# Kernel tuning notes

Hardware: AMD Instinct MI355X
Metric: run time of the kernel (lower is better)

The kernel has to match this reference:

```python
import jax, jax.numpy as jnp
import numpy as np

DIM = 384
WS = 7
NH = 12
N = WS * WS
B_ = 4096
HEAD_DIM = DIM // NH
SCALE = HEAD_DIM ** (-0.5)


def _relative_position_index(ws: int) -> np.ndarray:
    coords = np.stack(np.meshgrid(np.arange(ws), np.arange(ws), indexing='ij'))  # [2,ws,ws]
    cf = coords.reshape(2, -1)  # [2, N]
    rel = cf[:, :, None] - cf[:, None, :]  # [2, N, N]
    rel = rel.transpose(1, 2, 0).copy()
    rel[:, :, 0] += ws - 1
    rel[:, :, 1] += ws - 1
    rel[:, :, 0] *= 2 * ws - 1
    return rel.sum(-1).astype(np.int32)  # [N, N]


def setup_inputs() -> dict:
    key = jax.random.key(0)
    ks = jax.random.split(key, 6)
    x = jax.random.normal(ks[0], (B_, N, DIM), dtype=jnp.float32)
    qkv_w = jax.random.normal(ks[1], (3 * DIM, DIM), dtype=jnp.float32) * 0.02
    qkv_b = jnp.zeros((3 * DIM,), dtype=jnp.float32)
    proj_w = jax.random.normal(ks[2], (DIM, DIM), dtype=jnp.float32) * 0.02
    proj_b = jnp.zeros((DIM,), dtype=jnp.float32)
    bias_table = jax.random.normal(ks[3], ((2 * WS - 1) * (2 * WS - 1), NH), dtype=jnp.float32) * 0.02
    rel_index = jnp.asarray(_relative_position_index(WS))  # [N, N] int32
    return {"x": x, "qkv_w": qkv_w, "qkv_b": qkv_b, "proj_w": proj_w,
            "proj_b": proj_b, "bias_table": bias_table, "rel_index": rel_index}


def reference(x, qkv_w, qkv_b, proj_w, proj_b, bias_table, rel_index):
    b, n, c = x.shape
    qkv = x @ qkv_w.T + qkv_b  # [B_, N, 3C]
    qkv = qkv.reshape(b, n, 3, NH, HEAD_DIM).transpose(2, 0, 3, 1, 4)  # [3, B_, H, N, hd]
    q, k, v = qkv[0], qkv[1], qkv[2]
    q = q * SCALE
    attn = jnp.einsum('bhnd,bhmd->bhnm', q, k)  # [B_, H, N, N]
    # relative position bias gather: [N*N] -> [N, N, H] -> [H, N, N]
    bias = bias_table[rel_index.reshape(-1)].reshape(n, n, NH).transpose(2, 0, 1)
    attn = attn + bias[None]
    attn = jax.nn.softmax(attn, axis=-1)
    out = jnp.einsum('bhnm,bhmd->bhnd', attn, v)  # [B_, H, N, hd]
    out = out.transpose(0, 2, 1, 3).reshape(b, n, c)
    return out @ proj_w.T + proj_b
```

## Files before the change

kernel.cpp:

```cpp
#include <hip/hip_runtime.h>
#include <stdint.h>
#include <stddef.h>

#define DIM_C    384
#define NHEADS   12
#define SEQ      49
#define HEADD    32
#define NWIN     4096
#define MTOT     (NWIN * SEQ)
#define QKV_N    (3 * DIM_C)
#define ATTN_SCALE 0.17677669529663687f

typedef __bf16 bf16_t;
typedef __bf16 bf16x8 __attribute__((ext_vector_type(8)));
typedef __bf16 bf16x4 __attribute__((ext_vector_type(4)));
typedef float  f32x4  __attribute__((ext_vector_type(4)));

static_assert(sizeof(bf16x8) == 16, "bf16x8 must be 16B");

#define QKV_BYTES     ((size_t)MTOT * QKV_N * 2)
#define AOUT_BYTES    ((size_t)MTOT * DIM_C * 2)
#define BIAS_ELEMS    (NHEADS * SEQ * SEQ)
#define BIASF_BYTES   ((size_t)BIAS_ELEMS * 4)
#define QKVW_BF_BYTES ((size_t)QKV_N * DIM_C * 2)

__global__ void convert_f32_bf16_kernel(const float* __restrict__ src,
                                        bf16_t* __restrict__ dst, int n4) {
    int i = blockIdx.x * 256 + threadIdx.x;
    if (i < n4) {
        float4 v = ((const float4*)src)[i];
        bf16x4 t;
        t[0] = (bf16_t)v.x; t[1] = (bf16_t)v.y;
        t[2] = (bf16_t)v.z; t[3] = (bf16_t)v.w;
        ((bf16x4*)dst)[i] = t;
    }
}

__global__ void bias_expand_kernel(const float* __restrict__ table,
                                   const int* __restrict__ rel,
                                   float* __restrict__ bias_full) {
    int i = blockIdx.x * 256 + threadIdx.x;
    if (i < BIAS_ELEMS) {
        int h  = i / (SEQ * SEQ);
        int mn = i % (SEQ * SEQ);
        bias_full[i] = table[rel[mn] * NHEADS + h];
    }
}

template <bool A_BF16, bool OUT_BF16, int NT>
__global__ __launch_bounds__(256) void gemm_kernel(
    const void* __restrict__ Av, const bf16_t* __restrict__ Bw,
    const float* __restrict__ bias, void* __restrict__ Cv, int ldc) {
    __shared__ bf16_t As[128 * 40];
    __shared__ bf16_t Bs[128 * 40];

    const int tid  = threadIdx.x;
    const int lane = tid & 63;
    const int wave = tid >> 6;
    const int l15  = lane & 15;
    const int quad = lane >> 4;
    const int wm = (wave >> 1) * 64;
    const int wn = (wave & 1) * 64;

    const int cpx = gridDim.x >> 3;
    const int bid = blockIdx.x;
    const int wid = (bid & 7) * cpx + (bid >> 3);
    const size_t m0 = (size_t)(wid / NT) * 128;
    const int    n0 = (wid % NT) * 128;

    f32x4 acc[4][4];
#pragma unroll
    for (int i = 0; i < 4; i++)
#pragma unroll
        for (int j = 0; j < 4; j++) acc[i][j] = f32x4{0.f, 0.f, 0.f, 0.f};

    for (int kt = 0; kt < DIM_C / 32; ++kt) {
        const int k0 = kt * 32;
        __syncthreads();
        if constexpr (A_BF16) {
            const bf16_t* A = (const bf16_t*)Av;
#pragma unroll
            for (int i = 0; i < 2; i++) {
                int c = tid + i * 256;
                int row = c >> 2, kq = c & 3;
                bf16x8 v = *(const bf16x8*)(A + (m0 + row) * DIM_C + k0 + kq * 8);
                *(bf16x8*)(&As[row * 40 + kq * 8]) = v;
            }
        } else {
            const float* A = (const float*)Av;
#pragma unroll
            for (int i = 0; i < 4; i++) {
                int c = tid + i * 256;
                int row = c >> 3, kq = c & 7;
                float4 v = *(const float4*)(A + (m0 + row) * DIM_C + k0 + kq * 4);
                bf16x4 t;
                t[0] = (bf16_t)v.x; t[1] = (bf16_t)v.y;
                t[2] = (bf16_t)v.z; t[3] = (bf16_t)v.w;
                *(bf16x4*)(&As[row * 40 + kq * 4]) = t;
            }
        }
        {
#pragma unroll
            for (int i = 0; i < 2; i++) {
                int c = tid + i * 256;
                int row = c >> 2, kq = c & 3;
                bf16x8 v = *(const bf16x8*)(Bw + (size_t)(n0 + row) * DIM_C + k0 + kq * 8);
                *(bf16x8*)(&Bs[row * 40 + kq * 8]) = v;
            }
        }
        __syncthreads();
        bf16x8 af[4], bfr[4];
#pragma unroll
        for (int mi = 0; mi < 4; mi++)
            af[mi] = *(const bf16x8*)(&As[(wm + mi * 16 + l15) * 40 + quad * 8]);
#pragma unroll
        for (int ni = 0; ni < 4; ni++)
            bfr[ni] = *(const bf16x8*)(&Bs[(wn + ni * 16 + l15) * 40 + quad * 8]);
#pragma unroll
        for (int mi = 0; mi < 4; mi++)
#pragma unroll
            for (int ni = 0; ni < 4; ni++)
                acc[mi][ni] = __builtin_amdgcn_mfma_f32_16x16x32_bf16(
                    af[mi], bfr[ni], acc[mi][ni], 0, 0, 0);
    }
#pragma unroll
    for (int mi = 0; mi < 4; mi++) {
#pragma unroll
        for (int ni = 0; ni < 4; ni++) {
            int col = n0 + wn + ni * 16 + l15;
            float bc = bias[col];
#pragma unroll
            for (int r = 0; r < 4; r++) {
                size_t row = m0 + wm + mi * 16 + quad * 4 + r;
                float v = acc[mi][ni][r] + bc;
                if constexpr (OUT_BF16)
                    ((bf16_t*)Cv)[row * (size_t)ldc + col] = (bf16_t)v;
                else
                    ((float*)Cv)[row * (size_t)ldc + col] = v;
            }
        }
    }
}

__global__ __launch_bounds__(256) void attn_kernel(
    const bf16_t* __restrict__ qkv, const float* __restrict__ bias_full,
    bf16_t* __restrict__ aout) {
    __shared__ bf16_t Ps[4][64 * 72];

    const int b    = blockIdx.x;
    const int lane = threadIdx.x & 63;
    const int wave = threadIdx.x >> 6;
    const int l15  = lane & 15;
    const int quad = lane >> 4;
    const bf16_t* base = qkv + (size_t)b * SEQ * QKV_N;
    bf16_t* ps = &Ps[wave][0];

#pragma unroll 1
    for (int hi = 0; hi < 3; ++hi) {
        const int h = wave * 3 + hi;
        bf16x8 qf[4], kf[4];
#pragma unroll
        for (int mi = 0; mi < 4; mi++) {
            int row = mi * 16 + l15;
            if (row < SEQ) {
                qf[mi] = *(const bf16x8*)(base + (size_t)row * QKV_N + h * HEADD + quad * 8);
                kf[mi] = *(const bf16x8*)(base + (size_t)row * QKV_N + DIM_C + h * HEADD + quad * 8);
            } else {
                bf16x8 z;
#pragma unroll
                for (int j = 0; j < 8; j++) z[j] = (bf16_t)0.f;
                qf[mi] = z; kf[mi] = z;
            }
        }
        f32x4 S[4][4];
#pragma unroll
        for (int mi = 0; mi < 4; mi++)
#pragma unroll
            for (int ni = 0; ni < 4; ni++)
                S[mi][ni] = __builtin_amdgcn_mfma_f32_16x16x32_bf16(
                    qf[mi], kf[ni], f32x4{0.f, 0.f, 0.f, 0.f}, 0, 0, 0);
        const float* bh = bias_full + h * SEQ * SEQ;
#pragma unroll
        for (int mi = 0; mi < 4; mi++)
#pragma unroll
            for (int r = 0; r < 4; r++) {
                int m = mi * 16 + quad * 4 + r;
#pragma unroll
                for (int ni = 0; ni < 4; ni++) {
                    int n = ni * 16 + l15;
                    float s = S[mi][ni][r];
                    s = (m < SEQ && n < SEQ) ? s * ATTN_SCALE + bh[m * SEQ + n] : -1e30f;
                    S[mi][ni][r] = s;
                }
            }
#pragma unroll
        for (int mi = 0; mi < 4; mi++)
#pragma unroll
            for (int r = 0; r < 4; r++) {
                float mx = -1e30f;
#pragma unroll
                for (int ni = 0; ni < 4; ni++) mx = fmaxf(mx, S[mi][ni][r]);
#pragma unroll
                for (int off = 1; off < 16; off <<= 1)
                    mx = fmaxf(mx, __shfl_xor(mx, off, 64));
                float sum = 0.f;
#pragma unroll
                for (int ni = 0; ni < 4; ni++) {
                    float e = __expf(S[mi][ni][r] - mx);
                    S[mi][ni][r] = e;
                    sum += e;
                }
#pragma unroll
                for (int off = 1; off < 16; off <<= 1)
                    sum += __shfl_xor(sum, off, 64);
                float inv = 1.f / sum;
                int m = mi * 16 + quad * 4 + r;
#pragma unroll
                for (int ni = 0; ni < 4; ni++) {
                    int n = ni * 16 + l15;
                    ps[m * 72 + n] = (bf16_t)(S[mi][ni][r] * inv);
                }
            }
        bf16x8 vf[2][2];
#pragma unroll
        for (int ki = 0; ki < 2; ki++)
#pragma unroll
            for (int di = 0; di < 2; di++) {
#pragma unroll
                for (int j = 0; j < 8; j++) {
                    int k = ki * 32 + quad * 8 + j;
                    vf[ki][di][j] = (k < SEQ)
                        ? base[(size_t)k * QKV_N + 2 * DIM_C + h * HEADD + di * 16 + l15]
                        : (bf16_t)0.f;
                }
            }
        f32x4 O[4][2];
#pragma unroll
        for (int mi = 0; mi < 4; mi++)
#pragma unroll
            for (int di = 0; di < 2; di++) O[mi][di] = f32x4{0.f, 0.f, 0.f, 0.f};
#pragma unroll
        for (int mi = 0; mi < 4; mi++)
#pragma unroll
            for (int ki = 0; ki < 2; ki++) {
                bf16x8 pa = *(const bf16x8*)(ps + (mi * 16 + l15) * 72 + ki * 32 + quad * 8);
#pragma unroll
                for (int di = 0; di < 2; di++)
                    O[mi][di] = __builtin_amdgcn_mfma_f32_16x16x32_bf16(
                        pa, vf[ki][di], O[mi][di], 0, 0, 0);
            }
#pragma unroll
        for (int mi = 0; mi < 4; mi++)
#pragma unroll
            for (int di = 0; di < 2; di++)
#pragma unroll
                for (int r = 0; r < 4; r++) {
                    int m = mi * 16 + quad * 4 + r;
                    if (m < SEQ)
                        aout[((size_t)b * SEQ + m) * DIM_C + h * HEADD + di * 16 + l15] =
                            (bf16_t)O[mi][di][r];
                }
    }
}

extern "C" void kernel_launch(void* const* d_in, const int* in_sizes, int n_in,
                              void* d_out, int out_size, void* d_ws, size_t ws_size,
                              hipStream_t stream) {
    (void)in_sizes; (void)n_in; (void)out_size; (void)ws_size;
    const float* x      = (const float*)d_in[0];
    const float* qkv_w  = (const float*)d_in[1];
    const float* qkv_b  = (const float*)d_in[2];
    const float* proj_w = (const float*)d_in[3];
    const float* proj_b = (const float*)d_in[4];
    const float* btable = (const float*)d_in[5];
    const int*   rel    = (const int*)d_in[6];
    float* out = (float*)d_out;

    char* ws = (char*)d_ws;
    bf16_t* qkv        = (bf16_t*)ws;
    bf16_t* aout       = (bf16_t*)(ws + QKV_BYTES);
    float*  bias_full  = (float*)(ws + QKV_BYTES + AOUT_BYTES);
    bf16_t* qkv_w_bf   = (bf16_t*)(ws + QKV_BYTES + AOUT_BYTES + BIASF_BYTES);
    bf16_t* proj_w_bf  = (bf16_t*)(ws + QKV_BYTES + AOUT_BYTES + BIASF_BYTES + QKVW_BF_BYTES);

    convert_f32_bf16_kernel<<<(QKV_N * DIM_C / 4 + 255) / 256, 256, 0, stream>>>(
        qkv_w, qkv_w_bf, QKV_N * DIM_C / 4);
    convert_f32_bf16_kernel<<<(DIM_C * DIM_C / 4 + 255) / 256, 256, 0, stream>>>(
        proj_w, proj_w_bf, DIM_C * DIM_C / 4);
    bias_expand_kernel<<<(BIAS_ELEMS + 255) / 256, 256, 0, stream>>>(btable, rel, bias_full);

    gemm_kernel<false, true, QKV_N / 128><<<(MTOT / 128) * (QKV_N / 128), 256, 0, stream>>>(
        x, qkv_w_bf, qkv_b, qkv, QKV_N);
    attn_kernel<<<NWIN, 256, 0, stream>>>(qkv, bias_full, aout);
    gemm_kernel<true, false, DIM_C / 128><<<(MTOT / 128) * (DIM_C / 128), 256, 0, stream>>>(
        aout, proj_w_bf, proj_b, out, DIM_C);
}
```

Measured before the change: 1.476 ms.

## Write V transposed from QKV GEMM and map one wave per window-head

The QKV GEMM epilogue now writes Q and K to a compact 768-wide buffer and writes V transposed per window into a padded [window][channel][64] layout. That buffer is stored in the output allocation, and its padding positions are zeroed. The attention kernel now gives each wave one (window, head) pair across a swizzled grid instead of three heads per block. It loads V with vector reads instead of scalar strided gathers, and reads the relative-position bias from a pre-padded, fragment-ordered table with the mask folded in. The aim is to cut uncoalesced V loads and per-element bias and mask work, and to raise parallelism. The cost is scattered 2-byte stores in the GEMM epilogue and reuse of the output buffer as scratch.

```diff
diff --git a/kernel.cpp b/kernel.cpp
--- a/kernel.cpp
+++ b/kernel.cpp
@@ -18,10 +18,10 @@
 
 static_assert(sizeof(bf16x8) == 16, "bf16x8 must be 16B");
 
-#define QKV_BYTES     ((size_t)MTOT * QKV_N * 2)
+#define QK_BYTES      ((size_t)MTOT * 768 * 2)
+#define VT_BYTES      ((size_t)NWIN * 384 * 64 * 2)
 #define AOUT_BYTES    ((size_t)MTOT * DIM_C * 2)
-#define BIAS_ELEMS    (NHEADS * SEQ * SEQ)
-#define BIASF_BYTES   ((size_t)BIAS_ELEMS * 4)
+#define BIASL_BYTES   ((size_t)NHEADS * 64 * 64 * 4)
 #define QKVW_BF_BYTES ((size_t)QKV_N * DIM_C * 2)
 
 __global__ void convert_f32_bf16_kernel(const float* __restrict__ src,
@@ -38,19 +38,24 @@
 
 __global__ void bias_expand_kernel(const float* __restrict__ table,
                                    const int* __restrict__ rel,
-                                   float* __restrict__ bias_full) {
+                                   float* __restrict__ bias_l) {
     int i = blockIdx.x * 256 + threadIdx.x;
-    if (i < BIAS_ELEMS) {
-        int h  = i / (SEQ * SEQ);
-        int mn = i % (SEQ * SEQ);
-        bias_full[i] = table[rel[mn] * NHEADS + h];
-    }
-}
-
-template <bool A_BF16, bool OUT_BF16, int NT>
+    if (i < NHEADS * 64 * 64) {
+        int h  = i >> 12;
+        int mn = i & 4095;
+        int m = mn >> 6, n = mn & 63;
+        float v = -1e30f;
+        if (m < SEQ && n < SEQ) v = table[rel[m * SEQ + n] * NHEADS + h];
+        int l = n & 15, ni = n >> 4;
+        bias_l[((h * 64 + m) * 16 + l) * 4 + ni] = v;
+    }
+}
+
+template <bool A_BF16, int MODE, int NT>
 __global__ __launch_bounds__(256) void gemm_kernel(
     const void* __restrict__ Av, const bf16_t* __restrict__ Bw,
-    const float* __restrict__ bias, void* __restrict__ Cv, int ldc) {
+    const float* __restrict__ bias, void* __restrict__ C0,
+    bf16_t* __restrict__ vt, int ldc) {
     __shared__ bf16_t As[128 * 40];
     __shared__ bf16_t Bs[128 * 40];
 
@@ -123,144 +128,177 @@
                 acc[mi][ni] = __builtin_amdgcn_mfma_f32_16x16x32_bf16(
                     af[mi], bfr[ni], acc[mi][ni], 0, 0, 0);
     }
-#pragma unroll
-    for (int mi = 0; mi < 4; mi++) {
-#pragma unroll
-        for (int ni = 0; ni < 4; ni++) {
-            int col = n0 + wn + ni * 16 + l15;
-            float bc = bias[col];
-#pragma unroll
-            for (int r = 0; r < 4; r++) {
-                size_t row = m0 + wm + mi * 16 + quad * 4 + r;
-                float v = acc[mi][ni][r] + bc;
-                if constexpr (OUT_BF16)
-                    ((bf16_t*)Cv)[row * (size_t)ldc + col] = (bf16_t)v;
-                else
-                    ((float*)Cv)[row * (size_t)ldc + col] = v;
-            }
-        }
-    }
-}
-
-__global__ __launch_bounds__(256) void attn_kernel(
-    const bf16_t* __restrict__ qkv, const float* __restrict__ bias_full,
-    bf16_t* __restrict__ aout) {
+
+    if constexpr (MODE == 0) {
+        float* C = (float*)C0;
+#pragma unroll
+        for (int mi = 0; mi < 4; mi++)
+#pragma unroll
+            for (int ni = 0; ni < 4; ni++) {
+                int col = n0 + wn + ni * 16 + l15;
+                float bc = bias[col];
+#pragma unroll
+                for (int r = 0; r < 4; r++) {
+                    size_t row = m0 + wm + mi * 16 + quad * 4 + r;
+                    C[row * (size_t)ldc + col] = acc[mi][ni][r] + bc;
+                }
+            }
+    } else {
+        if (n0 < 768) {
+            bf16_t* qkc = (bf16_t*)C0;
+#pragma unroll
+            for (int mi = 0; mi < 4; mi++)
+#pragma unroll
+                for (int ni = 0; ni < 4; ni++) {
+                    int col = n0 + wn + ni * 16 + l15;
+                    float bc = bias[col];
+#pragma unroll
+                    for (int r = 0; r < 4; r++) {
+                        size_t row = m0 + wm + mi * 16 + quad * 4 + r;
+                        qkc[row * 768 + col] = (bf16_t)(acc[mi][ni][r] + bc);
+                    }
+                }
+        } else {
+#pragma unroll
+            for (int mi = 0; mi < 4; mi++)
+#pragma unroll
+                for (int ni = 0; ni < 4; ni++) {
+                    int col = n0 + wn + ni * 16 + l15;
+                    float bc = bias[col];
+                    int vcol = col - 768;
+#pragma unroll
+                    for (int r = 0; r < 4; r++) {
+                        uint32_t row = (uint32_t)(m0 + wm + mi * 16 + quad * 4 + r);
+                        uint32_t b = row / 49u;
+                        uint32_t s = row - b * 49u;
+                        vt[((size_t)b * 384 + vcol) * 64 + s] =
+                            (bf16_t)(acc[mi][ni][r] + bc);
+                    }
+                }
+            int b0 = (int)(m0 / 49);
+#pragma unroll 1
+            for (int bw = 0; bw < 4; ++bw) {
+                int b = b0 + bw;
+                if (b < NWIN && b * 49 < (int)(m0) + 128) {
+#pragma unroll 1
+                    for (int e = tid; e < 128 * 15; e += 256) {
+                        int cl = e / 15;
+                        int sp = 49 + (e - cl * 15);
+                        vt[((size_t)b * 384 + (n0 - 768) + cl) * 64 + sp] = (bf16_t)0.f;
+                    }
+                }
+            }
+        }
+    }
+}
+
+__global__ __launch_bounds__(256, 4) void attn_kernel(
+    const bf16_t* __restrict__ qk, const bf16_t* __restrict__ vt,
+    const float* __restrict__ bias_l, bf16_t* __restrict__ aout) {
     __shared__ bf16_t Ps[4][64 * 72];
 
-    const int b    = blockIdx.x;
     const int lane = threadIdx.x & 63;
     const int wave = threadIdx.x >> 6;
     const int l15  = lane & 15;
     const int quad = lane >> 4;
-    const bf16_t* base = qkv + (size_t)b * SEQ * QKV_N;
+    const int bid  = blockIdx.x;
+    const int wid  = (bid & 7) * ((NWIN * NHEADS / 4) / 8) + (bid >> 3);
+    const int gw   = wid * 4 + wave;
+    const int b    = gw / NHEADS;
+    const int h    = gw - b * NHEADS;
+
+    const bf16_t* qb = qk + (size_t)b * SEQ * 768 + h * HEADD;
+    const bf16_t* kb = qb + DIM_C;
+    const bf16_t* vb = vt + ((size_t)b * 384 + h * HEADD) * 64;
+    const float*  bh = bias_l + h * 4096;
     bf16_t* ps = &Ps[wave][0];
 
-#pragma unroll 1
-    for (int hi = 0; hi < 3; ++hi) {
-        const int h = wave * 3 + hi;
-        bf16x8 qf[4], kf[4];
-#pragma unroll
-        for (int mi = 0; mi < 4; mi++) {
-            int row = mi * 16 + l15;
-            if (row < SEQ) {
-                qf[mi] = *(const bf16x8*)(base + (size_t)row * QKV_N + h * HEADD + quad * 8);
-                kf[mi] = *(const bf16x8*)(base + (size_t)row * QKV_N + DIM_C + h * HEADD + quad * 8);
-            } else {
-                bf16x8 z;
-#pragma unroll
-                for (int j = 0; j < 8; j++) z[j] = (bf16_t)0.f;
-                qf[mi] = z; kf[mi] = z;
-            }
-        }
-        f32x4 S[4][4];
-#pragma unroll
-        for (int mi = 0; mi < 4; mi++)
-#pragma unroll
-            for (int ni = 0; ni < 4; ni++)
-                S[mi][ni] = __builtin_amdgcn_mfma_f32_16x16x32_bf16(
-                    qf[mi], kf[ni], f32x4{0.f, 0.f, 0.f, 0.f}, 0, 0, 0);
-        const float* bh = bias_full + h * SEQ * SEQ;
-#pragma unroll
-        for (int mi = 0; mi < 4; mi++)
+    bf16x8 qf[4], kf[4];
+#pragma unroll
+    for (int mi = 0; mi < 4; mi++) {
+        int row = mi * 16 + l15;
+        if (row < SEQ) {
+            qf[mi] = *(const bf16x8*)(qb + (size_t)row * 768 + quad * 8);
+            kf[mi] = *(const bf16x8*)(kb + (size_t)row * 768 + quad * 8);
+        } else {
+            bf16x8 z;
+#pragma unroll
+            for (int j = 0; j < 8; j++) z[j] = (bf16_t)0.f;
+            qf[mi] = z; kf[mi] = z;
+        }
+    }
+    f32x4 S[4][4];
+#pragma unroll
+    for (int mi = 0; mi < 4; mi++)
+#pragma unroll
+        for (int ni = 0; ni < 4; ni++)
+            S[mi][ni] = __builtin_amdgcn_mfma_f32_16x16x32_bf16(
+                qf[mi], kf[ni], f32x4{0.f, 0.f, 0.f, 0.f}, 0, 0, 0);
+#pragma unroll
+    for (int mi = 0; mi < 4; mi++)
+#pragma unroll
+        for (int r = 0; r < 4; r++) {
+            int m = mi * 16 + quad * 4 + r;
+            f32x4 bv = *(const f32x4*)(bh + ((m << 4) + l15) * 4);
+            float mx = -1e30f;
+#pragma unroll
+            for (int ni = 0; ni < 4; ni++) {
+                float s = S[mi][ni][r] * ATTN_SCALE + bv[ni];
+                S[mi][ni][r] = s;
+                mx = fmaxf(mx, s);
+            }
+#pragma unroll
+            for (int off = 1; off < 16; off <<= 1)
+                mx = fmaxf(mx, __shfl_xor(mx, off, 64));
+            float sum = 0.f;
+#pragma unroll
+            for (int ni = 0; ni < 4; ni++) {
+                float e = __expf(S[mi][ni][r] - mx);
+                S[mi][ni][r] = e;
+                sum += e;
+            }
+#pragma unroll
+            for (int off = 1; off < 16; off <<= 1)
+                sum += __shfl_xor(sum, off, 64);
+            float inv = 1.f / sum;
+#pragma unroll
+            for (int ni = 0; ni < 4; ni++) {
+                int n = ni * 16 + l15;
+                ps[m * 72 + n] = (bf16_t)(S[mi][ni][r] * inv);
+            }
+        }
+    bf16x8 vf[2][2];
+#pragma unroll
+    for (int ki = 0; ki < 2; ki++)
+#pragma unroll
+        for (int di = 0; di < 2; di++)
+            vf[ki][di] = *(const bf16x8*)(vb + (size_t)(di * 16 + l15) * 64 + ki * 32 + quad * 8);
+    f32x4 O[4][2];
+#pragma unroll
+    for (int mi = 0; mi < 4; mi++)
+#pragma unroll
+        for (int di = 0; di < 2; di++) O[mi][di] = f32x4{0.f, 0.f, 0.f, 0.f};
+#pragma unroll
+    for (int mi = 0; mi < 4; mi++)
+#pragma unroll
+        for (int ki = 0; ki < 2; ki++) {
+            bf16x8 pa = *(const bf16x8*)(ps + (mi * 16 + l15) * 72 + ki * 32 + quad * 8);
+#pragma unroll
+            for (int di = 0; di < 2; di++)
+                O[mi][di] = __builtin_amdgcn_mfma_f32_16x16x32_bf16(
+                    pa, vf[ki][di], O[mi][di], 0, 0, 0);
+        }
+#pragma unroll
+    for (int mi = 0; mi < 4; mi++)
+#pragma unroll
+        for (int di = 0; di < 2; di++)
 #pragma unroll
             for (int r = 0; r < 4; r++) {
                 int m = mi * 16 + quad * 4 + r;
-#pragma unroll
-                for (int ni = 0; ni < 4; ni++) {
-                    int n = ni * 16 + l15;
-                    float s = S[mi][ni][r];
-                    s = (m < SEQ && n < SEQ) ? s * ATTN_SCALE + bh[m * SEQ + n] : -1e30f;
-                    S[mi][ni][r] = s;
-                }
-            }
-#pragma unroll
-        for (int mi = 0; mi < 4; mi++)
-#pragma unroll
-            for (int r = 0; r < 4; r++) {
-                float mx = -1e30f;
-#pragma unroll
-                for (int ni = 0; ni < 4; ni++) mx = fmaxf(mx, S[mi][ni][r]);
-#pragma unroll
-                for (int off = 1; off < 16; off <<= 1)
-                    mx = fmaxf(mx, __shfl_xor(mx, off, 64));
-                float sum = 0.f;
-#pragma unroll
-                for (int ni = 0; ni < 4; ni++) {
-                    float e = __expf(S[mi][ni][r] - mx);
-                    S[mi][ni][r] = e;
-                    sum += e;
-                }
-#pragma unroll
-                for (int off = 1; off < 16; off <<= 1)
-                    sum += __shfl_xor(sum, off, 64);
-                float inv = 1.f / sum;
-                int m = mi * 16 + quad * 4 + r;
-#pragma unroll
-                for (int ni = 0; ni < 4; ni++) {
-                    int n = ni * 16 + l15;
-                    ps[m * 72 + n] = (bf16_t)(S[mi][ni][r] * inv);
-                }
-            }
-        bf16x8 vf[2][2];
-#pragma unroll
-        for (int ki = 0; ki < 2; ki++)
-#pragma unroll
-            for (int di = 0; di < 2; di++) {
-#pragma unroll
-                for (int j = 0; j < 8; j++) {
-                    int k = ki * 32 + quad * 8 + j;
-                    vf[ki][di][j] = (k < SEQ)
-                        ? base[(size_t)k * QKV_N + 2 * DIM_C + h * HEADD + di * 16 + l15]
-                        : (bf16_t)0.f;
-                }
-            }
-        f32x4 O[4][2];
-#pragma unroll
-        for (int mi = 0; mi < 4; mi++)
-#pragma unroll
-            for (int di = 0; di < 2; di++) O[mi][di] = f32x4{0.f, 0.f, 0.f, 0.f};
-#pragma unroll
-        for (int mi = 0; mi < 4; mi++)
-#pragma unroll
-            for (int ki = 0; ki < 2; ki++) {
-                bf16x8 pa = *(const bf16x8*)(ps + (mi * 16 + l15) * 72 + ki * 32 + quad * 8);
-#pragma unroll
-                for (int di = 0; di < 2; di++)
-                    O[mi][di] = __builtin_amdgcn_mfma_f32_16x16x32_bf16(
-                        pa, vf[ki][di], O[mi][di], 0, 0, 0);
-            }
-#pragma unroll
-        for (int mi = 0; mi < 4; mi++)
-#pragma unroll
-            for (int di = 0; di < 2; di++)
-#pragma unroll
-                for (int r = 0; r < 4; r++) {
-                    int m = mi * 16 + quad * 4 + r;
-                    if (m < SEQ)
-                        aout[((size_t)b * SEQ + m) * DIM_C + h * HEADD + di * 16 + l15] =
-                            (bf16_t)O[mi][di][r];
-                }
-    }
+                if (m < SEQ)
+                    aout[((size_t)b * SEQ + m) * DIM_C + h * HEADD + di * 16 + l15] =
+                        (bf16_t)O[mi][di][r];
+            }
 }
 
 extern "C" void kernel_launch(void* const* d_in, const int* in_sizes, int n_in,
@@ -277,21 +315,23 @@
     float* out = (float*)d_out;
 
     char* ws = (char*)d_ws;
-    bf16_t* qkv        = (bf16_t*)ws;
-    bf16_t* aout       = (bf16_t*)(ws + QKV_BYTES);
-    float*  bias_full  = (float*)(ws + QKV_BYTES + AOUT_BYTES);
-    bf16_t* qkv_w_bf   = (bf16_t*)(ws + QKV_BYTES + AOUT_BYTES + BIASF_BYTES);
-    bf16_t* proj_w_bf  = (bf16_t*)(ws + QKV_BYTES + AOUT_BYTES + BIASF_BYTES + QKVW_BF_BYTES);
+    bf16_t* qkbuf     = (bf16_t*)ws;
+    bf16_t* aout      = (bf16_t*)(ws + QK_BYTES);
+    float*  bias_l    = (float*)(ws + QK_BYTES + AOUT_BYTES);
+    bf16_t* qkv_w_bf  = (bf16_t*)(ws + QK_BYTES + AOUT_BYTES + BIASL_BYTES);
+    bf16_t* proj_w_bf = (bf16_t*)(ws + QK_BYTES + AOUT_BYTES + BIASL_BYTES + QKVW_BF_BYTES);
+    bf16_t* vt        = (bf16_t*)d_out;
 
     convert_f32_bf16_kernel<<<(QKV_N * DIM_C / 4 + 255) / 256, 256, 0, stream>>>(
         qkv_w, qkv_w_bf, QKV_N * DIM_C / 4);
     convert_f32_bf16_kernel<<<(DIM_C * DIM_C / 4 + 255) / 256, 256, 0, stream>>>(
         proj_w, proj_w_bf, DIM_C * DIM_C / 4);
-    bias_expand_kernel<<<(BIAS_ELEMS + 255) / 256, 256, 0, stream>>>(btable, rel, bias_full);
-
-    gemm_kernel<false, true, QKV_N / 128><<<(MTOT / 128) * (QKV_N / 128), 256, 0, stream>>>(
-        x, qkv_w_bf, qkv_b, qkv, QKV_N);
-    attn_kernel<<<NWIN, 256, 0, stream>>>(qkv, bias_full, aout);
-    gemm_kernel<true, false, DIM_C / 128><<<(MTOT / 128) * (DIM_C / 128), 256, 0, stream>>>(
-        aout, proj_w_bf, proj_b, out, DIM_C);
-}
+    bias_expand_kernel<<<(NHEADS * 64 * 64 + 255) / 256, 256, 0, stream>>>(
+        btable, rel, bias_l);
+
+    gemm_kernel<false, 1, QKV_N / 128><<<(MTOT / 128) * (QKV_N / 128), 256, 0, stream>>>(
+        x, qkv_w_bf, qkv_b, qkbuf, vt, 0);
+    attn_kernel<<<NWIN * NHEADS / 4, 256, 0, stream>>>(qkbuf, vt, bias_l, aout);
+    gemm_kernel<true, 0, DIM_C / 128><<<(MTOT / 128) * (DIM_C / 128), 256, 0, stream>>>(
+        aout, proj_w_bf, proj_b, out, nullptr, DIM_C);
+}
```

Result: faster. 1.330 ms (-9.9%).
